# Kernel tuning notes

Hardware: AMD Instinct MI355X
Metric: run time of the kernel (lower is better)

The kernel has to match this reference:

```python
import jax, jax.numpy as jnp
import numpy as np

N_NODES = 100000
N_EDGES = 3200000
N_FEAT = 128
EMB = 64
HID = 64
N_SUB = 500000
N_GRAPHS = 1024
BN_EPS = 1e-5


def setup_inputs() -> dict:
    key = jax.random.key(0)
    ks = jax.random.split(key, 12)
    full_x = jax.random.normal(ks[0], (N_NODES, N_FEAT), dtype=jnp.float32)
    full_edge_index = jax.random.randint(ks[1], (2, N_EDGES), 0, N_NODES, dtype=jnp.int64)
    subgraph_node_indices = jax.random.randint(ks[2], (N_SUB,), 0, N_NODES, dtype=jnp.int64)
    batch_vector = jax.random.randint(ks[3], (N_SUB,), 0, N_GRAPHS, dtype=jnp.int64)
    # GCNConv params (glorot-style scale)
    W_enc = jax.random.normal(ks[4], (N_FEAT, EMB), dtype=jnp.float32) * (1.0 / np.sqrt(N_FEAT))
    b_enc = jnp.zeros((EMB,), dtype=jnp.float32)
    # predictor MLP params
    W1 = jax.random.normal(ks[5], (EMB, HID), dtype=jnp.float32) * (1.0 / np.sqrt(EMB))
    b1 = jnp.zeros((HID,), dtype=jnp.float32)
    gamma = jnp.ones((HID,), dtype=jnp.float32)
    beta = jnp.zeros((HID,), dtype=jnp.float32)
    W2 = jax.random.normal(ks[6], (HID, 1), dtype=jnp.float32) * (1.0 / np.sqrt(HID))
    b2 = jnp.zeros((1,), dtype=jnp.float32)
    return {
        "full_x": full_x,
        "full_edge_index": full_edge_index,
        "subgraph_node_indices": subgraph_node_indices,
        "batch_vector": batch_vector,
        "W_enc": W_enc, "b_enc": b_enc,
        "W1": W1, "b1": b1, "gamma": gamma, "beta": beta,
        "W2": W2, "b2": b2,
    }


def gcn_conv(x, edge_index, W, b):
    # PyG GCNConv: add self-loops, symmetric degree normalization, linear transform
    n = x.shape[0]
    loops = jnp.arange(n, dtype=edge_index.dtype)
    row = jnp.concatenate([edge_index[0], loops])  # source
    col = jnp.concatenate([edge_index[1], loops])  # target
    deg = jax.ops.segment_sum(jnp.ones_like(col, dtype=x.dtype), col, num_segments=n)
    dinv = jnp.where(deg > 0, jax.lax.rsqrt(deg), 0.0)
    norm = dinv[row] * dinv[col]  # [E+N]
    xw = x @ W  # transform first: [N, EMB]
    msgs = xw[row] * norm[:, None]
    out = jax.ops.segment_sum(msgs, col, num_segments=n)
    return out + b


def reference(full_x, full_edge_index, subgraph_node_indices, batch_vector,
              W_enc, b_enc, W1, b1, gamma, beta, W2, b2):
    # encoder + relu over all nodes
    h = jax.nn.relu(gcn_conv(full_x, full_edge_index, W_enc, b_enc))  # [N, EMB]
    # gather subgraph members
    sub = h[subgraph_node_indices]  # [N_SUB, EMB]
    # segment-mean pool into per-subgraph embeddings
    sums = jax.ops.segment_sum(sub, batch_vector, num_segments=N_GRAPHS)
    cnts = jax.ops.segment_sum(jnp.ones((sub.shape[0],), sub.dtype), batch_vector, num_segments=N_GRAPHS)
    pooled = sums / jnp.maximum(cnts, 1.0)[:, None]  # [N_GRAPHS, EMB]
    # predictor: Linear -> ReLU -> BatchNorm1d (training-mode batch stats) -> Linear
    z = jax.nn.relu(pooled @ W1 + b1)  # [N_GRAPHS, HID]
    mu = jnp.mean(z, axis=0)
    var = jnp.mean((z - mu) ** 2, axis=0)  # biased, as torch BN normalization
    zn = (z - mu) * jax.lax.rsqrt(var + BN_EPS) * gamma + beta
    return zn @ W2 + b2  # [N_GRAPHS, 1]
```

## Files before the change

kernel.cpp:

```cpp
#include <hip/hip_runtime.h>

#define N_NODES 100000
#define N_EDGES 3200000
#define N_FEAT 128
#define EMB 64
#define HID 64
#define N_SUB 500000
#define N_GRAPHS 1024
#define BN_EPS 1e-5f

#define NBKT 782
#define TILE 4096
#define NTILES 782
#define NGTILES 123
#define BKT_CAP 7168
#define GCAP 640
#define ZROW 100000
#define RPT 9
#define GEMM_BLOCKS 2048
#define WSTRIDE 136

typedef __attribute__((ext_vector_type(8))) short short8;
typedef __attribute__((ext_vector_type(4))) float floatx4;

#define OFF_BCUR   0u
#define OFF_BCURG  4096u
#define OFF_BNSUM  8192u
#define ZERO_BYTES 8704u
#define OFF_DINV   12288u
#define OFF_OFFS   412672u
#define OFF_PAIRS  812672u
#define OFF_CSR    OFF_PAIRS
#define OFF_XWS    23235200u
#define OFF_SORTED 36035328u
#define OFF_H      38656768u
#define OFF_Z      51456896u

__device__ __forceinline__ bool is_bf(const unsigned* gamma_raw) {
  return (gamma_raw[0] & 0xFFFFu) != 0u;
}
__device__ __forceinline__ bool idx_is64(const int* subp) {
  return (subp[1] | subp[3] | subp[5] | subp[7]) == 0;
}
__device__ __forceinline__ float bf2f(ushort u) {
  union { unsigned i; float f; } v; v.i = ((unsigned)u) << 16; return v.f;
}
__device__ __forceinline__ ushort f2bf(float f) {
  union { float f; unsigned i; } v; v.f = f;
  unsigned lsb = (v.i >> 16) & 1u;
  v.i += 0x7FFFu + lsb;
  return (ushort)(v.i >> 16);
}
__device__ __forceinline__ float ld_f(const void* p, int i, bool bf) {
  return bf ? bf2f(((const ushort*)p)[i]) : ((const float*)p)[i];
}
__device__ __forceinline__ float lo_bf(unsigned d) {
  union { unsigned u; float f; } v; v.u = d << 16; return v.f;
}
__device__ __forceinline__ float hi_bf(unsigned d) {
  union { unsigned u; float f; } v; v.u = d & 0xFFFF0000u; return v.f;
}

__global__ __launch_bounds__(256) void k_scatsort(
    const int* e, const int* subp, const int* batch,
    int* bcur, unsigned* pairs, int* bcurg, int* sorted) {
  __shared__ int cnt[1024], lscan[1024], gbase[1024], wsum[4];
  __shared__ unsigned stage[TILE];
  __shared__ unsigned short stgb[TILE];
  bool w64 = idx_is64(subp);
  int tid = threadIdx.x, lane = tid & 63, wv = tid >> 6;
  bool edges = blockIdx.x < NTILES;
  int base = edges ? blockIdx.x * TILE : (blockIdx.x - NTILES) * TILE;
  int tot  = edges ? N_EDGES : N_SUB;
  int nb   = edges ? NBKT : N_GRAPHS;
  int tcnt = min(TILE, tot - base);
  int rem  = tcnt - wv * 1024;
  int key[16], val[16];
  int nv = 0;
  const int* kb = edges ? e : batch;
  const int* vb = edges ? e : subp;
  long long ko = edges ? (long long)N_EDGES : 0;
  if (w64) {
    const int4* kp = (const int4*)kb + (ko + base) / 2 + wv * 512 + lane;
    const int4* vp = (const int4*)vb + base / 2 + wv * 512 + lane;
#pragma unroll
    for (int k = 0; k < 8; ++k) {
      if ((k * 64 + lane) * 2 < rem) {
        int4 a = kp[k * 64];
        int4 c = vp[k * 64];
        key[2 * k] = a.x;     val[2 * k] = c.x;
        key[2 * k + 1] = a.z; val[2 * k + 1] = c.z;
        nv = 2 * k + 2;
      }
    }
  } else {
    const int4* kp = (const int4*)(kb + ko) + base / 4 + wv * 256 + lane;
    const int4* vp = (const int4*)vb + base / 4 + wv * 256 + lane;
#pragma unroll
    for (int k = 0; k < 4; ++k) {
      if ((k * 64 + lane) * 4 < rem) {
        int4 a = kp[k * 64];
        int4 c = vp[k * 64];
        key[4 * k] = a.x;     val[4 * k] = c.x;
        key[4 * k + 1] = a.y; val[4 * k + 1] = c.y;
        key[4 * k + 2] = a.z; val[4 * k + 2] = c.z;
        key[4 * k + 3] = a.w; val[4 * k + 3] = c.w;
        nv = 4 * k + 4;
      }
    }
  }
  for (int i = tid; i < 1024; i += 256) cnt[i] = 0;
  __syncthreads();
#pragma unroll
  for (int k = 0; k < 16; ++k)
    if (k < nv) atomicAdd(&cnt[edges ? (key[k] >> 7) : key[k]], 1);
  __syncthreads();
  int b0 = tid * 4;
  int v0 = cnt[b0], v1 = cnt[b0 + 1], v2 = cnt[b0 + 2], v3 = cnt[b0 + 3];
  int s = v0 + v1 + v2 + v3, sc = s;
#pragma unroll
  for (int d = 1; d < 64; d <<= 1) {
    int t = __shfl_up(sc, d);
    if (lane >= d) sc += t;
  }
  if (lane == 63) wsum[wv] = sc;
  __syncthreads();
  int woff = 0;
#pragma unroll
  for (int w = 0; w < 4; ++w) woff += (w < wv) ? wsum[w] : 0;
  int excl = sc + woff - s;
  lscan[b0] = excl; lscan[b0 + 1] = excl + v0;
  lscan[b0 + 2] = excl + v0 + v1; lscan[b0 + 3] = excl + v0 + v1 + v2;
  __syncthreads();
  for (int b = tid; b < 1024; b += 256) {
    int c = (b < nb) ? cnt[b] : 0;
    gbase[b] = c ? (edges ? b * BKT_CAP + atomicAdd(&bcur[b], c)
                          : b * GCAP + atomicAdd(&bcurg[b], c)) : 0;
  }
  __syncthreads();
  for (int b = tid; b < 1024; b += 256) cnt[b] = 0;
  __syncthreads();
#pragma unroll
  for (int k = 0; k < 16; ++k) {
    if (k < nv) {
      int b = edges ? (key[k] >> 7) : key[k];
      int r = atomicAdd(&cnt[b], 1);
      int p = lscan[b] + r;
      stage[p] = edges ? (((unsigned)(key[k] & 127) << 20) | (unsigned)val[k])
                       : (unsigned)val[k];
      stgb[p] = (unsigned short)b;
    }
  }
  __syncthreads();
  if (edges) {
    for (int j = tid; j < tcnt; j += 256) {
      int b = stgb[j];
      pairs[gbase[b] + (j - lscan[b])] = stage[j];
    }
  } else {
    for (int j = tid; j < tcnt; j += 256) {
      int b = stgb[j];
      sorted[gbase[b] + (j - lscan[b])] = (int)stage[j];
    }
  }
}

__global__ __launch_bounds__(512) void k_csr(
    const unsigned* __restrict__ pairs, const int* __restrict__ bcur,
    int* __restrict__ csr, unsigned* __restrict__ offs, float* __restrict__ dinv) {
  __shared__ int dl[128], loff[128], lcur[128];
  __shared__ int stage[BKT_CAP];
  __shared__ int ptot;
  int tid = threadIdx.x, b = blockIdx.x;
  if (tid < 128) dl[tid] = 0;
  __syncthreads();
  int s = b * BKT_CAP, cnt = bcur[b];
  unsigned pr[RPT];
#pragma unroll
  for (int k = 0; k < RPT; ++k) {
    int j = tid + k * 512;
    pr[k] = (j < cnt) ? pairs[s + j] : 0u;
  }
#pragma unroll
  for (int k = 0; k < RPT; ++k)
    if (tid + k * 512 < cnt) atomicAdd(&dl[pr[k] >> 20], 1);
  __syncthreads();
  int deg = 0, pd = 0;
  if (tid < 128) { deg = dl[tid]; pd = (deg + 31) & ~31; loff[tid] = pd; }
  __syncthreads();
  for (int d = 1; d < 128; d <<= 1) {
    int t = (tid >= d && tid < 128) ? loff[tid - d] : 0;
    __syncthreads();
    if (tid < 128) loff[tid] += t;
    __syncthreads();
  }
  if (tid < 128) {
    int excl = loff[tid] - pd;
    lcur[tid] = excl;
    int n = b * 128 + tid;
    if (n < N_NODES) {
      offs[n] = ((unsigned)(pd >> 5) << 24) | (unsigned)(s + excl);
      dinv[n] = rsqrtf((float)(deg + 1));
    }
    if (tid == 127) ptot = loff[127];
  }
  __syncthreads();
  int pt = ptot;
  for (int j = tid; j < pt; j += 512) stage[j] = ZROW;
  __syncthreads();
#pragma unroll
  for (int k = 0; k < RPT; ++k) {
    if (tid + k * 512 < cnt) {
      int pos = atomicAdd(&lcur[pr[k] >> 20], 1);
      stage[pos] = (int)(pr[k] & 0xFFFFF);
    }
  }
  __syncthreads();
  for (int j = tid; j < pt; j += 512) csr[s + j] = stage[j];
}

__global__ __launch_bounds__(256) void k_gemm(
    const void* xraw, const void* Wraw, const unsigned* gamu,
    const float* __restrict__ dinv, ushort* __restrict__ xws) {
  __shared__ ushort swT[64 * WSTRIDE];
  __shared__ ushort sx[4][16 * 128];
  if (blockIdx.x == 0 && threadIdx.x < 32)
    ((unsigned*)xws)[(unsigned)ZROW * 32u + threadIdx.x] = 0u;
  bool bf = is_bf(gamu);
  int tid = threadIdx.x;
  if (bf) {
    const unsigned* W2 = (const unsigned*)Wraw;
    for (int i = tid; i < N_FEAT * EMB / 2; i += 256) {
      unsigned w2 = W2[i];
      int k = i >> 5;
      int c = (i & 31) * 2;
      swT[c * WSTRIDE + k]       = (ushort)(w2 & 0xFFFFu);
      swT[(c + 1) * WSTRIDE + k] = (ushort)(w2 >> 16);
    }
  } else {
    const float* Wf = (const float*)Wraw;
    for (int i = tid; i < N_FEAT * EMB; i += 256) {
      int k = i >> 6, c = i & 63;
      swT[c * WSTRIDE + k] = f2bf(Wf[i]);
    }
  }
  __syncthreads();
  int wv = tid >> 6, lane = tid & 63;
  int m = lane & 15, quad = lane >> 4;
  int c0 = wv * 16;
  short8 bfrag[4];
#pragma unroll
  for (int kc = 0; kc < 4; ++kc)
    bfrag[kc] = *(const short8*)(swT + (c0 + m) * WSTRIDE + kc * 32 + quad * 8);
  const ushort* xs = (const ushort*)xraw;
  const float*  xf = (const float*)xraw;
  ushort* mysx = &sx[wv][0];
  for (int t = blockIdx.x; t < N_NODES / 16; t += GEMM_BLOCKS) {
    int r0 = t * 16;
    if (bf) {
      const uint4* src = (const uint4*)(xs + r0 * N_FEAT);
#pragma unroll
      for (int j = 0; j < 4; ++j) {
        int g = j * 64 + lane;
        int row = g >> 4, col = g & 15;
        uint4 v = src[g];
        *(uint4*)(mysx + row * 128 + ((col ^ (row & 7)) << 3)) = v;
      }
    } else {
      const float4* src = (const float4*)(xf + r0 * N_FEAT);
#pragma unroll
      for (int j = 0; j < 8; ++j) {
        int g = j * 64 + lane;
        int row = g >> 5, fc = g & 31;
        float4 v = src[g];
        unsigned u0 = (unsigned)f2bf(v.x) | ((unsigned)f2bf(v.y) << 16);
        unsigned u1 = (unsigned)f2bf(v.z) | ((unsigned)f2bf(v.w) << 16);
        uint2 w; w.x = u0; w.y = u1;
        *(uint2*)(mysx + row * 128 + ((((fc >> 1) ^ (row & 7)) << 3) + (fc & 1) * 4)) = w;
      }
    }
    floatx4 acc0 = {0.f, 0.f, 0.f, 0.f}, acc1 = {0.f, 0.f, 0.f, 0.f};
    short8 a0 = *(const short8*)(mysx + m * 128 + (((0 * 4 + quad) ^ (m & 7)) << 3));
    short8 a1 = *(const short8*)(mysx + m * 128 + (((1 * 4 + quad) ^ (m & 7)) << 3));
    short8 a2 = *(const short8*)(mysx + m * 128 + (((2 * 4 + quad) ^ (m & 7)) << 3));
    short8 a3 = *(const short8*)(mysx + m * 128 + (((3 * 4 + quad) ^ (m & 7)) << 3));
    acc0 = __builtin_amdgcn_mfma_f32_16x16x32_bf16(a0, bfrag[0], acc0, 0, 0, 0);
    acc1 = __builtin_amdgcn_mfma_f32_16x16x32_bf16(a1, bfrag[1], acc1, 0, 0, 0);
    acc0 = __builtin_amdgcn_mfma_f32_16x16x32_bf16(a2, bfrag[2], acc0, 0, 0, 0);
    acc1 = __builtin_amdgcn_mfma_f32_16x16x32_bf16(a3, bfrag[3], acc1, 0, 0, 0);
    floatx4 acc = acc0 + acc1;
    float4 dv = *(const float4*)(dinv + r0 + quad * 4);
#pragma unroll
    for (int r = 0; r < 4; ++r) {
      int row = r0 + quad * 4 + r;
      float d = (r == 0) ? dv.x : (r == 1) ? dv.y : (r == 2) ? dv.z : dv.w;
      xws[row * EMB + c0 + m] = f2bf(acc[r] * d);
    }
  }
}

#define ACCA(d) { aL0 += lo_bf(d.x); aH0 += hi_bf(d.x); aL1 += lo_bf(d.y); aH1 += hi_bf(d.y); \
                  aL2 += lo_bf(d.z); aH2 += hi_bf(d.z); aL3 += lo_bf(d.w); aH3 += hi_bf(d.w); }
#define ACCB(d) { bL0 += lo_bf(d.x); bH0 += hi_bf(d.x); bL1 += lo_bf(d.y); bH1 += hi_bf(d.y); \
                  bL2 += lo_bf(d.z); bH2 += hi_bf(d.z); bL3 += lo_bf(d.w); bH3 += hi_bf(d.w); }

__global__ __launch_bounds__(256) void k_agg(
    const ushort* __restrict__ xws, const float* __restrict__ dinv,
    const unsigned* __restrict__ offs, const int* __restrict__ csr,
    const void* benc, const unsigned* gamu, ushort* __restrict__ h) {
  if (blockIdx.x == 0 && threadIdx.x < 32)
    ((unsigned*)h)[(unsigned)ZROW * 32u + threadIdx.x] = 0u;
  bool bf = is_bf(gamu);
  const uint4* xw4 = (const uint4*)xws;
  int wv = threadIdx.x >> 6, lane = threadIdx.x & 63;
  int e8 = lane >> 3, q = lane & 7;
  int nA = blockIdx.x * 8 + wv, nB = nA + 4;
  unsigned wA = offs[nA], wB = offs[nB];
  int stA = (int)(wA & 0xFFFFFFu), iA = (int)(wA >> 24);
  int stB = (int)(wB & 0xFFFFFFu), iB = (int)(wB >> 24);
  float aL0 = 0.f, aH0 = 0.f, aL1 = 0.f, aH1 = 0.f,
        aL2 = 0.f, aH2 = 0.f, aL3 = 0.f, aH3 = 0.f;
  float bL0 = 0.f, bH0 = 0.f, bL1 = 0.f, bH1 = 0.f,
        bL2 = 0.f, bH2 = 0.f, bL3 = 0.f, bH3 = 0.f;
  const int4* ipA = (const int4*)(csr + stA) + e8;
  const int4* ipB = (const int4*)(csr + stB) + e8;
  int im = min(iA, iB), it = 0;
  for (; it < im; ++it) {
    int4 ja = ipA[it * 8];
    int4 jb = ipB[it * 8];
    uint4 a0 = xw4[ja.x * 8 + q];
    uint4 a1 = xw4[ja.y * 8 + q];
    uint4 a2 = xw4[ja.z * 8 + q];
    uint4 a3 = xw4[ja.w * 8 + q];
    uint4 c0 = xw4[jb.x * 8 + q];
    uint4 c1 = xw4[jb.y * 8 + q];
    uint4 c2 = xw4[jb.z * 8 + q];
    uint4 c3 = xw4[jb.w * 8 + q];
    ACCA(a0) ACCA(a1) ACCA(a2) ACCA(a3)
    ACCB(c0) ACCB(c1) ACCB(c2) ACCB(c3)
  }
  for (; it < iA; ++it) {
    int4 ja = ipA[it * 8];
    uint4 a0 = xw4[ja.x * 8 + q];
    uint4 a1 = xw4[ja.y * 8 + q];
    uint4 a2 = xw4[ja.z * 8 + q];
    uint4 a3 = xw4[ja.w * 8 + q];
    ACCA(a0) ACCA(a1) ACCA(a2) ACCA(a3)
  }
  for (int jt = im; jt < iB; ++jt) {
    int4 jb = ipB[jt * 8];
    uint4 c0 = xw4[jb.x * 8 + q];
    uint4 c1 = xw4[jb.y * 8 + q];
    uint4 c2 = xw4[jb.z * 8 + q];
    uint4 c3 = xw4[jb.w * 8 + q];
    ACCB(c0) ACCB(c1) ACCB(c2) ACCB(c3)
  }
#pragma unroll
  for (int msk = 8; msk < 64; msk <<= 1) {
    aL0 += __shfl_xor(aL0, msk); aH0 += __shfl_xor(aH0, msk);
    aL1 += __shfl_xor(aL1, msk); aH1 += __shfl_xor(aH1, msk);
    aL2 += __shfl_xor(aL2, msk); aH2 += __shfl_xor(aH2, msk);
    aL3 += __shfl_xor(aL3, msk); aH3 += __shfl_xor(aH3, msk);
    bL0 += __shfl_xor(bL0, msk); bH0 += __shfl_xor(bH0, msk);
    bL1 += __shfl_xor(bL1, msk); bH1 += __shfl_xor(bH1, msk);
    bL2 += __shfl_xor(bL2, msk); bH2 += __shfl_xor(bH2, msk);
    bL3 += __shfl_xor(bL3, msk); bH3 += __shfl_xor(bH3, msk);
  }
  if (e8 == 0) {
    float dnA = dinv[nA], dnB = dinv[nB];
    uint4 usA = xw4[nA * 8 + q];
    uint4 usB = xw4[nB * 8 + q];
    float be0 = ld_f(benc, q * 8 + 0, bf), be1 = ld_f(benc, q * 8 + 1, bf);
    float be2 = ld_f(benc, q * 8 + 2, bf), be3 = ld_f(benc, q * 8 + 3, bf);
    float be4 = ld_f(benc, q * 8 + 4, bf), be5 = ld_f(benc, q * 8 + 5, bf);
    float be6 = ld_f(benc, q * 8 + 6, bf), be7 = ld_f(benc, q * 8 + 7, bf);
    ushort o[8];
    uint4 ov;
    o[0] = f2bf(fmaxf((aL0 + lo_bf(usA.x)) * dnA + be0, 0.f));
    o[1] = f2bf(fmaxf((aH0 + hi_bf(usA.x)) * dnA + be1, 0.f));
    o[2] = f2bf(fmaxf((aL1 + lo_bf(usA.y)) * dnA + be2, 0.f));
    o[3] = f2bf(fmaxf((aH1 + hi_bf(usA.y)) * dnA + be3, 0.f));
    o[4] = f2bf(fmaxf((aL2 + lo_bf(usA.z)) * dnA + be4, 0.f));
    o[5] = f2bf(fmaxf((aH2 + hi_bf(usA.z)) * dnA + be5, 0.f));
    o[6] = f2bf(fmaxf((aL3 + lo_bf(usA.w)) * dnA + be6, 0.f));
    o[7] = f2bf(fmaxf((aH3 + hi_bf(usA.w)) * dnA + be7, 0.f));
    ov.x = (unsigned)o[0] | ((unsigned)o[1] << 16);
    ov.y = (unsigned)o[2] | ((unsigned)o[3] << 16);
    ov.z = (unsigned)o[4] | ((unsigned)o[5] << 16);
    ov.w = (unsigned)o[6] | ((unsigned)o[7] << 16);
    ((uint4*)h)[nA * 8 + q] = ov;
    o[0] = f2bf(fmaxf((bL0 + lo_bf(usB.x)) * dnB + be0, 0.f));
    o[1] = f2bf(fmaxf((bH0 + hi_bf(usB.x)) * dnB + be1, 0.f));
    o[2] = f2bf(fmaxf((bL1 + lo_bf(usB.y)) * dnB + be2, 0.f));
    o[3] = f2bf(fmaxf((bH1 + hi_bf(usB.y)) * dnB + be3, 0.f));
    o[4] = f2bf(fmaxf((bL2 + lo_bf(usB.z)) * dnB + be4, 0.f));
    o[5] = f2bf(fmaxf((bH2 + hi_bf(usB.z)) * dnB + be5, 0.f));
    o[6] = f2bf(fmaxf((bL3 + lo_bf(usB.w)) * dnB + be6, 0.f));
    o[7] = f2bf(fmaxf((bH3 + hi_bf(usB.w)) * dnB + be7, 0.f));
    ov.x = (unsigned)o[0] | ((unsigned)o[1] << 16);
    ov.y = (unsigned)o[2] | ((unsigned)o[3] << 16);
    ov.z = (unsigned)o[4] | ((unsigned)o[5] << 16);
    ov.w = (unsigned)o[6] | ((unsigned)o[7] << 16);
    ((uint4*)h)[nB * 8 + q] = ov;
  }
}

__global__ void k_poolmlp1(const ushort* __restrict__ h, const int* __restrict__ sorted,
                           const int* __restrict__ bcurg, const void* W1, const void* b1,
                           const unsigned* gamu, float* __restrict__ z, float* bn) {
  bool bf = is_bf(gamu);
  __shared__ float red[4 * 64];
  __shared__ float pl[64];
  const uint4* h4 = (const uint4*)h;
  int g = blockIdx.x;
  int tid = threadIdx.x, wv = tid >> 6, lane = tid & 63;
  int e8 = lane >> 3, q = lane & 7;
  int start = g * GCAP, cnt = bcurg[g];
  int end = start + cnt;
  float aL0 = 0.f, aH0 = 0.f, aL1 = 0.f, aH1 = 0.f, aL2 = 0.f, aH2 = 0.f, aL3 = 0.f, aH3 = 0.f;
  for (int i = start + wv * 32; i < end; i += 128) {
#pragma unroll
    for (int c = 0; c < 4; ++c) {
      int idx = i + c * 8 + e8;
      int l = sorted[idx];
      int nn = (idx < end) ? l : ZROW;
      uint4 u = h4[nn * 8 + q];
      ACCA(u)
    }
  }
#pragma unroll
  for (int msk = 8; msk < 64; msk <<= 1) {
    aL0 += __shfl_xor(aL0, msk); aH0 += __shfl_xor(aH0, msk);
    aL1 += __shfl_xor(aL1, msk); aH1 += __shfl_xor(aH1, msk);
    aL2 += __shfl_xor(aL2, msk); aH2 += __shfl_xor(aH2, msk);
    aL3 += __shfl_xor(aL3, msk); aH3 += __shfl_xor(aH3, msk);
  }
  if (e8 == 0) {
    float* r = red + wv * 64 + q * 8;
    r[0] = aL0; r[1] = aH0; r[2] = aL1; r[3] = aH1;
    r[4] = aL2; r[5] = aH2; r[6] = aL3; r[7] = aH3;
  }
  __syncthreads();
  if (tid < 64) {
    float s = red[tid] + red[64 + tid] + red[128 + tid] + red[192 + tid];
    pl[tid] = s / fmaxf((float)cnt, 1.f);
  }
  __syncthreads();
  if (tid < 64) {
    int f = tid;
    float acc = ld_f(b1, f, bf);
#pragma unroll 8
    for (int k = 0; k < HID; ++k) acc += pl[k] * ld_f(W1, k * HID + f, bf);
    float zv = fmaxf(acc, 0.f);
    z[g * HID + f] = zv;
    atomicAdd(&bn[f], zv);
    atomicAdd(&bn[HID + f], zv * zv);
  }
}

__global__ void k_mlp2(const float* __restrict__ z, const float* __restrict__ bn,
                       const void* gmm, const void* beta, const void* W2, const void* b2,
                       const unsigned* gamu, void* out) {
  bool bf = is_bf(gamu);
  int wv = threadIdx.x >> 6, f = threadIdx.x & 63;
  int g = blockIdx.x * 4 + wv;
  float mu = bn[f] * (1.f / N_GRAPHS);
  float var = bn[HID + f] * (1.f / N_GRAPHS) - mu * mu;
  float zn = (z[g * HID + f] - mu) * rsqrtf(var + BN_EPS) * ld_f(gmm, f, bf) + ld_f(beta, f, bf);
  float val = zn * ld_f(W2, f, bf);
  for (int off = 32; off; off >>= 1) val += __shfl_down(val, off);
  if (f == 0) {
    val += ld_f(b2, 0, bf);
    if (bf) ((ushort*)out)[g] = f2bf(val);
    else    ((float*)out)[g]  = val;
  }
}

extern "C" void kernel_launch(void* const* d_in, const int* in_sizes, int n_in,
                              void* d_out, int out_size, void* d_ws, size_t ws_size,
                              hipStream_t stream) {
  const void* x_raw    = d_in[0];
  const int*  e_raw    = (const int*)d_in[1];
  const int*  sub_raw  = (const int*)d_in[2];
  const int*  bat_raw  = (const int*)d_in[3];
  const void* Wenc     = d_in[4];
  const void* benc     = d_in[5];
  const void* W1       = d_in[6];
  const void* b1       = d_in[7];
  const unsigned* gamu = (const unsigned*)d_in[8];
  const void* beta     = d_in[9];
  const void* W2       = d_in[10];
  const void* b2       = d_in[11];

  char* ws = (char*)d_ws;
  int*      bcur   = (int*)(ws + OFF_BCUR);
  int*      bcurg  = (int*)(ws + OFF_BCURG);
  float*    bnsum  = (float*)(ws + OFF_BNSUM);
  float*    dinv   = (float*)(ws + OFF_DINV);
  unsigned* offs   = (unsigned*)(ws + OFF_OFFS);
  unsigned* pairs  = (unsigned*)(ws + OFF_PAIRS);
  int*      csr    = (int*)(ws + OFF_CSR);
  ushort*   xws    = (ushort*)(ws + OFF_XWS);
  int*      sorted = (int*)(ws + OFF_SORTED);
  ushort*   h      = (ushort*)(ws + OFF_H);
  float*    z      = (float*)(ws + OFF_Z);

  hipMemsetAsync(ws, 0, ZERO_BYTES, stream);

  k_scatsort<<<NTILES + NGTILES, 256, 0, stream>>>(e_raw, sub_raw, bat_raw,
                                                   bcur, pairs, bcurg, sorted);
  k_csr     <<<NBKT, 512, 0, stream>>>(pairs, bcur, csr, offs, dinv);
  k_gemm    <<<GEMM_BLOCKS, 256, 0, stream>>>(x_raw, Wenc, gamu, dinv, xws);
  k_agg     <<<N_NODES / 8, 256, 0, stream>>>(xws, dinv, offs, csr, benc, gamu, h);
  k_poolmlp1<<<N_GRAPHS, 256, 0, stream>>>(h, sorted, bcurg, W1, b1, gamu, z, bnsum);
  k_mlp2    <<<N_GRAPHS / 4, 256, 0, stream>>>(z, bnsum, gamu, beta, W2, b2, gamu, d_out);
}
```

Baseline: 267.3 us.

## Merge GEMM into scatter-sort kernel and defer dinv scaling to CSR kernel

```diff
diff --git a/kernel.cpp b/kernel.cpp
--- a/kernel.cpp
+++ b/kernel.cpp
@@ -18,6 +18,8 @@
 #define ZROW 100000
 #define RPT 9
 #define GEMM_BLOCKS 2048
+#define SORT_BLOCKS (NTILES + NGTILES)
+#define PRE_BLOCKS (SORT_BLOCKS + GEMM_BLOCKS)
 #define WSTRIDE 136
 
 typedef __attribute__((ext_vector_type(8))) short short8;
@@ -35,6 +37,7 @@
 #define OFF_SORTED 36035328u
 #define OFF_H      38656768u
 #define OFF_Z      51456896u
+#define OFF_XWRAW  67108864u
 
 __device__ __forceinline__ bool is_bf(const unsigned* gamma_raw) {
   return (gamma_raw[0] & 0xFFFFu) != 0u;
@@ -61,14 +64,96 @@
   union { unsigned u; float f; } v; v.u = d & 0xFFFF0000u; return v.f;
 }
 
-__global__ __launch_bounds__(256) void k_scatsort(
-    const int* e, const int* subp, const int* batch,
-    int* bcur, unsigned* pairs, int* bcurg, int* sorted) {
-  __shared__ int cnt[1024], lscan[1024], gbase[1024], wsum[4];
-  __shared__ unsigned stage[TILE];
-  __shared__ unsigned short stgb[TILE];
+__global__ __launch_bounds__(256) void k_pre(
+    const void* xraw, const int* e, const int* subp, const int* batch,
+    const void* Wraw, const unsigned* gamu,
+    int* bcur, unsigned* pairs, int* bcurg, int* sorted,
+    float* __restrict__ xwraw, ushort* xws ) {
+  __shared__ __align__(16) char smem[36880];
+  int tid = threadIdx.x, lane = tid & 63, wv = tid >> 6;
+
+  if (blockIdx.x >= SORT_BLOCKS) {
+    ushort* swT = (ushort*)smem;
+    ushort* sxa = (ushort*)(smem + 17408);
+    if (blockIdx.x == SORT_BLOCKS && tid < 32)
+      ((unsigned*)xws)[(unsigned)ZROW * 32u + tid] = 0u;
+    bool bf = is_bf(gamu);
+    if (bf) {
+      const unsigned* W2 = (const unsigned*)Wraw;
+      for (int i = tid; i < N_FEAT * EMB / 2; i += 256) {
+        unsigned w2 = W2[i];
+        int k = i >> 5;
+        int c = (i & 31) * 2;
+        swT[c * WSTRIDE + k]       = (ushort)(w2 & 0xFFFFu);
+        swT[(c + 1) * WSTRIDE + k] = (ushort)(w2 >> 16);
+      }
+    } else {
+      const float* Wf = (const float*)Wraw;
+      for (int i = tid; i < N_FEAT * EMB; i += 256) {
+        int k = i >> 6, c = i & 63;
+        swT[c * WSTRIDE + k] = f2bf(Wf[i]);
+      }
+    }
+    __syncthreads();
+    int m = lane & 15, quad = lane >> 4;
+    int c0 = wv * 16;
+    short8 bfrag[4];
+#pragma unroll
+    for (int kc = 0; kc < 4; ++kc)
+      bfrag[kc] = *(const short8*)(swT + (c0 + m) * WSTRIDE + kc * 32 + quad * 8);
+    const ushort* xs = (const ushort*)xraw;
+    const float*  xf = (const float*)xraw;
+    ushort* mysx = sxa + wv * 2048;
+    for (int t = blockIdx.x - SORT_BLOCKS; t < N_NODES / 16; t += GEMM_BLOCKS) {
+      int r0 = t * 16;
+      if (bf) {
+        const uint4* src = (const uint4*)(xs + r0 * N_FEAT);
+#pragma unroll
+        for (int j = 0; j < 4; ++j) {
+          int g = j * 64 + lane;
+          int row = g >> 4, col = g & 15;
+          uint4 v = src[g];
+          *(uint4*)(mysx + row * 128 + ((col ^ (row & 7)) << 3)) = v;
+        }
+      } else {
+        const float4* src = (const float4*)(xf + r0 * N_FEAT);
+#pragma unroll
+        for (int j = 0; j < 8; ++j) {
+          int g = j * 64 + lane;
+          int row = g >> 5, fc = g & 31;
+          float4 v = src[g];
+          unsigned u0 = (unsigned)f2bf(v.x) | ((unsigned)f2bf(v.y) << 16);
+          unsigned u1 = (unsigned)f2bf(v.z) | ((unsigned)f2bf(v.w) << 16);
+          uint2 w; w.x = u0; w.y = u1;
+          *(uint2*)(mysx + row * 128 + ((((fc >> 1) ^ (row & 7)) << 3) + (fc & 1) * 4)) = w;
+        }
+      }
+      floatx4 acc0 = {0.f, 0.f, 0.f, 0.f}, acc1 = {0.f, 0.f, 0.f, 0.f};
+      short8 a0 = *(const short8*)(mysx + m * 128 + (((0 * 4 + quad) ^ (m & 7)) << 3));
+      short8 a1 = *(const short8*)(mysx + m * 128 + (((1 * 4 + quad) ^ (m & 7)) << 3));
+      short8 a2 = *(const short8*)(mysx + m * 128 + (((2 * 4 + quad) ^ (m & 7)) << 3));
+      short8 a3 = *(const short8*)(mysx + m * 128 + (((3 * 4 + quad) ^ (m & 7)) << 3));
+      acc0 = __builtin_amdgcn_mfma_f32_16x16x32_bf16(a0, bfrag[0], acc0, 0, 0, 0);
+      acc1 = __builtin_amdgcn_mfma_f32_16x16x32_bf16(a1, bfrag[1], acc1, 0, 0, 0);
+      acc0 = __builtin_amdgcn_mfma_f32_16x16x32_bf16(a2, bfrag[2], acc0, 0, 0, 0);
+      acc1 = __builtin_amdgcn_mfma_f32_16x16x32_bf16(a3, bfrag[3], acc1, 0, 0, 0);
+      floatx4 acc = acc0 + acc1;
+#pragma unroll
+      for (int r = 0; r < 4; ++r) {
+        int row = r0 + quad * 4 + r;
+        xwraw[row * EMB + c0 + m] = acc[r];
+      }
+    }
+    return;
+  }
+
+  int*      cnt   = (int*)smem;
+  int*      lscan = (int*)(smem + 4096);
+  int*      gbase = (int*)(smem + 8192);
+  int*      wsum  = (int*)(smem + 12288);
+  unsigned* stage = (unsigned*)(smem + 12304);
+  unsigned short* stgb = (unsigned short*)(smem + 28688);
   bool w64 = idx_is64(subp);
-  int tid = threadIdx.x, lane = tid & 63, wv = tid >> 6;
   bool edges = blockIdx.x < NTILES;
   int base = edges ? blockIdx.x * TILE : (blockIdx.x - NTILES) * TILE;
   int tot  = edges ? N_EDGES : N_SUB;
@@ -167,8 +252,10 @@
 
 __global__ __launch_bounds__(512) void k_csr(
     const unsigned* __restrict__ pairs, const int* __restrict__ bcur,
-    int* __restrict__ csr, unsigned* __restrict__ offs, float* __restrict__ dinv) {
+    int* __restrict__ csr, unsigned* __restrict__ offs, float* __restrict__ dinv,
+    const float* __restrict__ xwraw, ushort* __restrict__ xws) {
   __shared__ int dl[128], loff[128], lcur[128];
+  __shared__ float sdinv[128];
   __shared__ int stage[BKT_CAP];
   __shared__ int ptot;
   int tid = threadIdx.x, b = blockIdx.x;
@@ -197,14 +284,34 @@
   if (tid < 128) {
     int excl = loff[tid] - pd;
     lcur[tid] = excl;
+    float dv = rsqrtf((float)(deg + 1));
+    sdinv[tid] = dv;
     int n = b * 128 + tid;
     if (n < N_NODES) {
       offs[n] = ((unsigned)(pd >> 5) << 24) | (unsigned)(s + excl);
-      dinv[n] = rsqrtf((float)(deg + 1));
+      dinv[n] = dv;
     }
     if (tid == 127) ptot = loff[127];
   }
   __syncthreads();
+  {
+    size_t nb0 = (size_t)b * 128;
+    const float4* xr4 = (const float4*)(xwraw + nb0 * EMB);
+    uint2* xo2 = (uint2*)(xws + nb0 * EMB);
+#pragma unroll
+    for (int k = 0; k < 4; ++k) {
+      int idx = k * 512 + tid;
+      int row = idx >> 4;
+      if (b * 128 + row < N_NODES) {
+        float4 v = xr4[idx];
+        float d = sdinv[row];
+        uint2 w;
+        w.x = (unsigned)f2bf(v.x * d) | ((unsigned)f2bf(v.y * d) << 16);
+        w.y = (unsigned)f2bf(v.z * d) | ((unsigned)f2bf(v.w * d) << 16);
+        xo2[idx] = w;
+      }
+    }
+  }
   int pt = ptot;
   for (int j = tid; j < pt; j += 512) stage[j] = ZROW;
   __syncthreads();
@@ -217,86 +324,6 @@
   }
   __syncthreads();
   for (int j = tid; j < pt; j += 512) csr[s + j] = stage[j];
-}
-
-__global__ __launch_bounds__(256) void k_gemm(
-    const void* xraw, const void* Wraw, const unsigned* gamu,
-    const float* __restrict__ dinv, ushort* __restrict__ xws) {
-  __shared__ ushort swT[64 * WSTRIDE];
-  __shared__ ushort sx[4][16 * 128];
-  if (blockIdx.x == 0 && threadIdx.x < 32)
-    ((unsigned*)xws)[(unsigned)ZROW * 32u + threadIdx.x] = 0u;
-  bool bf = is_bf(gamu);
-  int tid = threadIdx.x;
-  if (bf) {
-    const unsigned* W2 = (const unsigned*)Wraw;
-    for (int i = tid; i < N_FEAT * EMB / 2; i += 256) {
-      unsigned w2 = W2[i];
-      int k = i >> 5;
-      int c = (i & 31) * 2;
-      swT[c * WSTRIDE + k]       = (ushort)(w2 & 0xFFFFu);
-      swT[(c + 1) * WSTRIDE + k] = (ushort)(w2 >> 16);
-    }
-  } else {
-    const float* Wf = (const float*)Wraw;
-    for (int i = tid; i < N_FEAT * EMB; i += 256) {
-      int k = i >> 6, c = i & 63;
-      swT[c * WSTRIDE + k] = f2bf(Wf[i]);
-    }
-  }
-  __syncthreads();
-  int wv = tid >> 6, lane = tid & 63;
-  int m = lane & 15, quad = lane >> 4;
-  int c0 = wv * 16;
-  short8 bfrag[4];
-#pragma unroll
-  for (int kc = 0; kc < 4; ++kc)
-    bfrag[kc] = *(const short8*)(swT + (c0 + m) * WSTRIDE + kc * 32 + quad * 8);
-  const ushort* xs = (const ushort*)xraw;
-  const float*  xf = (const float*)xraw;
-  ushort* mysx = &sx[wv][0];
-  for (int t = blockIdx.x; t < N_NODES / 16; t += GEMM_BLOCKS) {
-    int r0 = t * 16;
-    if (bf) {
-      const uint4* src = (const uint4*)(xs + r0 * N_FEAT);
-#pragma unroll
-      for (int j = 0; j < 4; ++j) {
-        int g = j * 64 + lane;
-        int row = g >> 4, col = g & 15;
-        uint4 v = src[g];
-        *(uint4*)(mysx + row * 128 + ((col ^ (row & 7)) << 3)) = v;
-      }
-    } else {
-      const float4* src = (const float4*)(xf + r0 * N_FEAT);
-#pragma unroll
-      for (int j = 0; j < 8; ++j) {
-        int g = j * 64 + lane;
-        int row = g >> 5, fc = g & 31;
-        float4 v = src[g];
-        unsigned u0 = (unsigned)f2bf(v.x) | ((unsigned)f2bf(v.y) << 16);
-        unsigned u1 = (unsigned)f2bf(v.z) | ((unsigned)f2bf(v.w) << 16);
-        uint2 w; w.x = u0; w.y = u1;
-        *(uint2*)(mysx + row * 128 + ((((fc >> 1) ^ (row & 7)) << 3) + (fc & 1) * 4)) = w;
-      }
-    }
-    floatx4 acc0 = {0.f, 0.f, 0.f, 0.f}, acc1 = {0.f, 0.f, 0.f, 0.f};
-    short8 a0 = *(const short8*)(mysx + m * 128 + (((0 * 4 + quad) ^ (m & 7)) << 3));
-    short8 a1 = *(const short8*)(mysx + m * 128 + (((1 * 4 + quad) ^ (m & 7)) << 3));
-    short8 a2 = *(const short8*)(mysx + m * 128 + (((2 * 4 + quad) ^ (m & 7)) << 3));
-    short8 a3 = *(const short8*)(mysx + m * 128 + (((3 * 4 + quad) ^ (m & 7)) << 3));
-    acc0 = __builtin_amdgcn_mfma_f32_16x16x32_bf16(a0, bfrag[0], acc0, 0, 0, 0);
-    acc1 = __builtin_amdgcn_mfma_f32_16x16x32_bf16(a1, bfrag[1], acc1, 0, 0, 0);
-    acc0 = __builtin_amdgcn_mfma_f32_16x16x32_bf16(a2, bfrag[2], acc0, 0, 0, 0);
-    acc1 = __builtin_amdgcn_mfma_f32_16x16x32_bf16(a3, bfrag[3], acc1, 0, 0, 0);
-    floatx4 acc = acc0 + acc1;
-    float4 dv = *(const float4*)(dinv + r0 + quad * 4);
-#pragma unroll
-    for (int r = 0; r < 4; ++r) {
-      int row = r0 + quad * 4 + r;
-      float d = (r == 0) ? dv.x : (r == 1) ? dv.y : (r == 2) ? dv.z : dv.w;
-      xws[row * EMB + c0 + m] = f2bf(acc[r] * d);
-    }
-  }
 }
 
 #define ACCA(d) { aL0 += lo_bf(d.x); aH0 += hi_bf(d.x); aL1 += lo_bf(d.y); aH1 += hi_bf(d.y); \
@@ -504,13 +531,14 @@
   int*      sorted = (int*)(ws + OFF_SORTED);
   ushort*   h      = (ushort*)(ws + OFF_H);
   float*    z      = (float*)(ws + OFF_Z);
+  float*    xwraw  = (float*)(ws + OFF_XWRAW);
 
   hipMemsetAsync(ws, 0, ZERO_BYTES, stream);
 
-  k_scatsort<<<NTILES + NGTILES, 256, 0, stream>>>(e_raw, sub_raw, bat_raw,
-                                                   bcur, pairs, bcurg, sorted);
-  k_csr     <<<NBKT, 512, 0, stream>>>(pairs, bcur, csr, offs, dinv);
-  k_gemm    <<<GEMM_BLOCKS, 256, 0, stream>>>(x_raw, Wenc, gamu, dinv, xws);
+  k_pre     <<<PRE_BLOCKS, 256, 0, stream>>>(x_raw, e_raw, sub_raw, bat_raw,
+                                             Wenc, gamu, bcur, pairs, bcurg,
+                                             sorted, xwraw, xws);
+  k_csr     <<<NBKT, 512, 0, stream>>>(pairs, bcur, csr, offs, dinv, xwraw, xws);
   k_agg     <<<N_NODES / 8, 256, 0, stream>>>(xws, dinv, offs, csr, benc, gamu, h);
   k_poolmlp1<<<N_GRAPHS, 256, 0, stream>>>(h, sorted, bcurg, W1, b1, gamu, z, bnsum);
   k_mlp2    <<<N_GRAPHS / 4, 256, 0, stream>>>(z, bnsum, gamu, beta, W2, b2, gamu, d_out);
```

Result: slower. 274.4 us (+2.6%).
